# Kernel optimization log

Hardware: AMD Instinct MI355X
Metric: run time of the kernel (lower is better)

Reference implementation:

```python
import jax, jax.numpy as jnp
from jax import lax
import numpy as np

B, H, W = 1, 128, 256
C = 32           # feature_channels
D = 32           # max_disp
HID = 64         # hidden_channels in message passing
ITERS = 5


def conv2d(x, w, b):
    # x: [N, Cin, H, W], w: [Cout, Cin, kh, kw], SAME padding, stride 1
    y = lax.conv_general_dilated(x, w, (1, 1), [(1, 1), (1, 1)],
                                 dimension_numbers=('NCHW', 'OIHW', 'NCHW'))
    return y + b[None, :, None, None]


def setup_inputs() -> dict:
    key = jax.random.key(0)
    ks = jax.random.split(key, 12)
    def p(k, shape, s=0.05):
        return jax.random.normal(k, shape, jnp.float32) * s
    return {
        'left_img':  jax.random.normal(ks[0], (B, 3, H, W), jnp.float32),
        'right_img': jax.random.normal(ks[1], (B, 3, H, W), jnp.float32),
        # feature extractor (3 -> C -> C)
        'fe_w1': p(ks[2], (C, 3, 3, 3)),  'fe_b1': jnp.zeros((C,), jnp.float32),
        'fe_w2': p(ks[3], (C, C, 3, 3)),  'fe_b2': jnp.zeros((C,), jnp.float32),
        # cost volume 1x1 conv over concat(left, shifted_right): 2C -> 1
        'cv_w': p(ks[4], (2 * C,)),       'cv_b': jnp.zeros((), jnp.float32),
        # message passing: concat(feature, belief)=C+1 -> HID -> 1
        'mp_w1': p(ks[5], (HID, C + 1, 3, 3)), 'mp_b1': jnp.zeros((HID,), jnp.float32),
        'mp_w2': p(ks[6], (1, HID, 3, 3)),     'mp_b2': jnp.zeros((1,), jnp.float32),
        # refinement: concat(left_img, disparity)=4 -> 32 -> 32 -> 1 residual
        'rf_w1': p(ks[7], (32, 4, 3, 3)),  'rf_b1': jnp.zeros((32,), jnp.float32),
        'rf_w2': p(ks[8], (32, 32, 3, 3)), 'rf_b2': jnp.zeros((32,), jnp.float32),
        'rf_w3': p(ks[9], (1, 32, 3, 3)),  'rf_b3': jnp.zeros((1,), jnp.float32),
    }


def _forward(left_img, right_img, fe_w1, fe_b1, fe_w2, fe_b2, cv_w, cv_b,
             mp_w1, mp_b1, mp_w2, mp_b2, rf_w1, rf_b1, rf_w2, rf_b2, rf_w3, rf_b3):
    def feat(img):
        h = jax.nn.relu(conv2d(img, fe_w1, fe_b1))
        return jax.nn.relu(conv2d(h, fe_w2, fe_b2))

    lf = feat(left_img)    # [B, C, H, W]
    rf = feat(right_img)   # [B, C, H, W]

    # Cost volume: shift right features by each disparity, 1x1 conv on concat.
    rf_sh = jnp.stack([jnp.pad(rf, ((0, 0), (0, 0), (0, 0), (d, 0)))[..., :W]
                       for d in range(D)])                     # [D, B, C, H, W]
    pair = jnp.concatenate([jnp.broadcast_to(lf[None], rf_sh.shape), rf_sh], axis=2)  # [D,B,2C,H,W]
    cost = jnp.einsum('dbchw,c->dbhw', pair, cv_w) + cv_b      # [D, B, H, W]
    data = cost[:, :, None]                                     # [D, B, 1, H, W]

    # Iterative BP message passing, vectorized across all disparity planes.
    def mp(data_term):  # data_term: [B, 1, H, W]
        def step(belief, _):
            x = jnp.concatenate([lf, belief], axis=1)           # [B, C+1, H, W]
            hdn = jax.nn.relu(conv2d(x, mp_w1, mp_b1))          # [B, HID, H, W]
            msg = conv2d(hdn, mp_w2, mp_b2)                     # [B, 1, H, W]
            return data_term + msg, None
        belief, _ = lax.scan(step, data_term, None, length=ITERS)
        return belief

    beliefs = jax.vmap(mp)(data)                                # [D, B, 1, H, W]
    refined = jnp.transpose(beliefs, (1, 2, 0, 3, 4))           # [B, 1, D, H, W]

    prob = jax.nn.softmax(-refined, axis=2)                     # [B, 1, D, H, W]
    idx = jnp.arange(D, dtype=prob.dtype)
    disparity = jnp.einsum('bodhw,d->bohw', prob, idx)          # [B, 1, H, W]

    # Refinement network (residual).
    x = jnp.concatenate([left_img, disparity], axis=1)          # [B, 4, H, W]
    r = jax.nn.relu(conv2d(x, rf_w1, rf_b1))
    r = jax.nn.relu(conv2d(r, rf_w2, rf_b2))
    res = conv2d(r, rf_w3, rf_b3)
    return disparity + res                                      # [B, 1, H, W]


def reference(left_img, right_img, fe_w1, fe_b1, fe_w2, fe_b2, cv_w, cv_b,
              mp_w1, mp_b1, mp_w2, mp_b2, rf_w1, rf_b1, rf_w2, rf_b2, rf_w3, rf_b3):
    return _forward(left_img, right_img, fe_w1, fe_b1, fe_w2, fe_b2, cv_w, cv_b,
                    mp_w1, mp_b1, mp_w2, mp_b2, rf_w1, rf_b1, rf_w2, rf_b2, rf_w3, rf_b3)
```

## Files before the change

kernel.cpp:

```cpp
#include <hip/hip_runtime.h>
#include <hip/hip_bf16.h>

#define H 128
#define W 256
#define HW (H*W)
#define NC 32
#define ND 32
#define NHID 64

__global__ __launch_bounds__(256) void conv3x3(
        const float* __restrict__ in0, const float* __restrict__ in1,
        float* __restrict__ out0, float* __restrict__ out1,
        const float* __restrict__ w, const float* __restrict__ b,
        int CIN, int COUT, int wstride, int dorelu,
        const float* __restrict__ addin) {
    __shared__ float wS[2304];
    __shared__ float tile[2][4][10][35];
    const int tid = threadIdx.x;
    const int zg = (COUT + 7) >> 3;
    const int img = blockIdx.z / zg;
    const int cog = blockIdx.z % zg;
    const float* in = img ? in1 : in0;
    float* out = img ? out1 : out0;
    const int cobase = cog * 8;
    int nco = COUT - cobase; if (nco > 8) nco = 8;
    const int gx0 = blockIdx.x * 32, gy0 = blockIdx.y * 8;
    const int tx = tid & 31, ty = tid >> 5;

    const int wcnt = nco * CIN * 9;
    for (int i = tid; i < wcnt; i += 256) {
        int co = i / (CIN * 9), rem = i % (CIN * 9);
        wS[i] = w[(size_t)(cobase + co) * wstride + rem];
    }

    const int nst = (CIN + 3) >> 2;
    {
        int nch = CIN < 4 ? CIN : 4;
        for (int i = tid; i < nch * 340; i += 256) {
            int ch = i / 340, rem = i % 340;
            int r = rem / 34, cc = rem % 34;
            int gy = gy0 + r - 1, gx = gx0 + cc - 1;
            tile[0][ch][r][cc] = (gy >= 0 && gy < H && gx >= 0 && gx < W)
                                 ? in[(size_t)ch * HW + gy * W + gx] : 0.f;
        }
    }
    __syncthreads();

    float acc[8];
#pragma unroll
    for (int i = 0; i < 8; i++) acc[i] = 0.f;

    for (int s = 0; s < nst; s++) {
        const int c0 = s * 4;
        int nch = CIN - c0; if (nch > 4) nch = 4;
        if (s + 1 < nst) {
            const int c1 = c0 + 4;
            int nch2 = CIN - c1; if (nch2 > 4) nch2 = 4;
            const int nb = (s + 1) & 1;
            for (int i = tid; i < nch2 * 340; i += 256) {
                int ch = i / 340, rem = i % 340;
                int r = rem / 34, cc = rem % 34;
                int gy = gy0 + r - 1, gx = gx0 + cc - 1;
                tile[nb][ch][r][cc] = (gy >= 0 && gy < H && gx >= 0 && gx < W)
                                      ? in[(size_t)(c1 + ch) * HW + gy * W + gx] : 0.f;
            }
        }
        const int cb = s & 1;
        for (int ch = 0; ch < nch; ch++) {
            float v[9];
#pragma unroll
            for (int ky = 0; ky < 3; ky++)
#pragma unroll
                for (int kx = 0; kx < 3; kx++)
                    v[ky * 3 + kx] = tile[cb][ch][ty + ky][tx + kx];
            const int wb = (c0 + ch) * 9;
#pragma unroll
            for (int co = 0; co < 8; co++) {
                if (co < nco) {
                    const float* wp = &wS[co * CIN * 9 + wb];
#pragma unroll
                    for (int k = 0; k < 9; k++) acc[co] += wp[k] * v[k];
                }
            }
        }
        __syncthreads();
    }

    const int gy = gy0 + ty, gx = gx0 + tx;
    const float ad = addin ? addin[gy * W + gx] : 0.f;
#pragma unroll
    for (int co = 0; co < 8; co++) {
        if (co < nco) {
            float r = acc[co] + b[cobase + co];
            if (dorelu) r = fmaxf(r, 0.f);
            r += ad;
            out[(size_t)(cobase + co) * HW + gy * W + gx] = r;
        }
    }
}

__global__ void chan_dot(const float* __restrict__ lf, const float* __restrict__ rf,
                         const float* __restrict__ cvw,
                         float* __restrict__ lsum, float* __restrict__ rsum) {
    int p = blockIdx.x * 256 + threadIdx.x;
    if (p >= HW) return;
    float ls = 0.f, rs = 0.f;
    for (int c = 0; c < NC; c++) {
        ls += lf[c * HW + p] * cvw[c];
        rs += rf[c * HW + p] * cvw[NC + c];
    }
    lsum[p] = ls;
    rsum[p] = rs;
}

__global__ void cost_expand(const float* __restrict__ lsum, const float* __restrict__ rsum,
                            const float* __restrict__ cvb,
                            float* __restrict__ cost, float* __restrict__ bel) {
    int idx = blockIdx.x * 256 + threadIdx.x;
    if (idx >= ND * HW) return;
    int d = idx / HW, p = idx % HW;
    int col = p & (W - 1);
    float c = lsum[p] + cvb[0];
    if (col >= d) c += rsum[p - d];
    cost[idx] = c;
    bel[idx] = c;
}

__global__ void a_transpose(const float* __restrict__ A, float* __restrict__ At) {
    __shared__ float t[64][65];
    int p0 = blockIdx.x * 64;
    int tx = threadIdx.x & 63;
    int ty = threadIdx.x >> 6;
#pragma unroll
    for (int r = 0; r < 16; r++) {
        int hid = ty * 16 + r;
        t[tx][hid] = A[(size_t)hid * HW + p0 + tx];
    }
    __syncthreads();
#pragma unroll
    for (int r = 0; r < 16; r++) {
        int p = ty * 16 + r;
        At[(size_t)(p0 + p) * 64 + tx] = t[p][tx];
    }
}

#define LOADROW(YC, AR)                                                        \
  {                                                                            \
    if ((YC) >= 0 && (YC) < H) {                                               \
      AR[0] = bp[e0off];                                                       \
      _Pragma("unroll") for (int j = 1; j < 17; j++) AR[j] = bp[(j - 8) * 64]; \
      AR[17] = bp[e17off];                                                     \
    }                                                                          \
    bp += W * 64;                                                              \
  }

#define COMPUTE(U, AR, HARR)                                                   \
  {                                                                            \
    const int yc_ = y0 + (U);                                                  \
    if (yc_ < 0 || yc_ >= H) {                                                 \
      _Pragma("unroll") for (int j = 0; j < 18; j++) HARR[j] = 0.f;            \
    } else {                                                                   \
      float bw_[3][3];                                                         \
      _Pragma("unroll") for (int r = 0; r < 3; r++) {                          \
        bw_[r][0] = belW[(U) + 1 + r][0];                                      \
        bw_[r][1] = belW[(U) + 1 + r][1];                                      \
      }                                                                        \
      _Pragma("unroll") for (int j = 0; j < 18; j++) {                         \
        float acc_ = AR[j];                                                    \
        _Pragma("unroll") for (int r = 0; r < 3; r++)                          \
          bw_[r][(j + 2) % 3] = belW[(U) + 1 + r][j + 2];                      \
        _Pragma("unroll") for (int r = 0; r < 3; r++)                          \
          _Pragma("unroll") for (int c = 0; c < 3; c++)                        \
            acc_ += w1[r * 3 + c] * bw_[r][(j + c) % 3];                       \
        HARR[j] = fmaxf(acc_, 0.f);                                            \
      }                                                                        \
      if (x0 == 0) HARR[0] = 0.f;                                              \
      if (x0 == W - 16) HARR[17] = 0.f;                                        \
    }                                                                          \
  }

#define EMIT3(T, HH2, HH1, HH0)                                                \
  {                                                                            \
    _Pragma("unroll") for (int jo = 0; jo < 16; jo++) {                        \
      float pp = w2[0] * HH2[jo] + w2[1] * HH2[jo + 1] + w2[2] * HH2[jo + 2]   \
               + w2[3] * HH1[jo] + w2[4] * HH1[jo + 1] + w2[5] * HH1[jo + 2]   \
               + w2[6] * HH0[jo] + w2[7] * HH0[jo + 1] + w2[8] * HH0[jo + 2];  \
      partW[jo][lane] = pp;                                                    \
    }                                                                          \
    asm volatile("s_waitcnt lgkmcnt(0)" ::: "memory");                         \
    {                                                                          \
      const float4* pr = (const float4*)&partW[pq][qq * 16];                   \
      float4 v0 = pr[0], v1 = pr[1], v2 = pr[2], v3 = pr[3];                   \
      float s_ = (((v0.x + v0.y) + (v0.z + v0.w)) +                            \
                  ((v1.x + v1.y) + (v1.z + v1.w))) +                           \
                 (((v2.x + v2.y) + (v2.z + v2.w)) +                            \
                  ((v3.x + v3.y) + (v3.z + v3.w)));                            \
      s_ += __shfl_xor(s_, 16);                                                \
      s_ += __shfl_xor(s_, 32);                                                \
      if (qq == 0)                                                             \
        bout[obase + (size_t)(T) * W] = costW[(T)][pq] + s_ + b2;              \
      asm volatile("s_waitcnt lgkmcnt(0)" ::: "memory");                       \
    }                                                                          \
  }

#define STEP(T, AIN, AOUT, HX2, HX1, HX0, DOLOAD)                              \
  {                                                                            \
    if (DOLOAD) { LOADROW(y0 + (T) + 2, AOUT); }                               \
    COMPUTE((T) + 1, AIN, HX0);                                                \
    EMIT3(T, HX2, HX1, HX0);                                                   \
  }

__global__ __launch_bounds__(256, 1) void mp_iter_fast(
    const float* __restrict__ At,
    const float* __restrict__ cost,
    const float* __restrict__ bin,
    float* __restrict__ bout,
    const float* __restrict__ mp_w1,
    const float* __restrict__ mp_w2,
    const float* __restrict__ mp_b2) {
    __shared__ float belS[4][20][20];
    __shared__ float costS[4][16][16];
    __shared__ float partS[4][16][68];

    const int tid = threadIdx.x;
    const int lane = tid & 63;
    const int lw = tid >> 6;
    float (*belW)[20]  = belS[lw];
    float (*costW)[16] = costS[lw];
    float (*partW)[68] = partS[lw];

    const int i = blockIdx.x;
    const int xcd = i & 7;
    const int jj = i >> 3;
    const int sl = jj & 15;
    const int d4 = jj >> 4;
    const int strip = xcd * 16 + sl;
    const int d = d4 * 4 + lw;
    const int x0 = (strip & 15) * 16;
    const int y0 = (strip >> 4) * 16;

    float w1[9], w2[9];
#pragma unroll
    for (int k = 0; k < 9; k++) {
        w1[k] = mp_w1[lane * 297 + 288 + k];
        w2[k] = mp_w2[lane * 9 + k];
    }
    const float b2 = mp_b2[0];

    const float* bp = At + (size_t)(y0 - 1) * (W * 64) + (x0 + 7) * 64 + lane;
    const int e0off  = (x0 == 0)      ? -448 : -512;
    const int e17off = (x0 == W - 16) ?  512 :  576;

    const float* beld = bin + (size_t)d * HW;
#pragma unroll
    for (int it = 0; it < 7; it++) {
        int idx = it * 64 + lane;
        if (idx < 400) {
            int r = idx / 20, c = idx % 20;
            int gy = y0 - 2 + r, gx = x0 - 2 + c;
            belW[r][c] = (gy >= 0 && gy < H && gx >= 0 && gx < W) ? beld[gy * W + gx] : 0.f;
        }
    }
#pragma unroll
    for (int it = 0; it < 4; it++) {
        int idx = it * 64 + lane;
        int r = idx >> 4, c = idx & 15;
        costW[r][c] = cost[(size_t)d * HW + (size_t)(y0 + r) * W + x0 + c];
    }
    asm volatile("s_waitcnt lgkmcnt(0)" ::: "memory");

    const int pq = lane & 15, qq = lane >> 4;
    const size_t obase = (size_t)d * HW + (size_t)y0 * W + x0 + pq;

    float aA[18], aB[18];
    float hA[18], hB[18], hC[18];

    LOADROW(y0 - 1, aA);
    LOADROW(y0, aB);
    COMPUTE(-1, aA, hA);
    LOADROW(y0 + 1, aA);
    COMPUTE(0, aB, hB);

    STEP(0,  aA, aB, hA, hB, hC, 1)
    STEP(1,  aB, aA, hB, hC, hA, 1)
    STEP(2,  aA, aB, hC, hA, hB, 1)
    STEP(3,  aB, aA, hA, hB, hC, 1)
    STEP(4,  aA, aB, hB, hC, hA, 1)
    STEP(5,  aB, aA, hC, hA, hB, 1)
    STEP(6,  aA, aB, hA, hB, hC, 1)
    STEP(7,  aB, aA, hB, hC, hA, 1)
    STEP(8,  aA, aB, hC, hA, hB, 1)
    STEP(9,  aB, aA, hA, hB, hC, 1)
    STEP(10, aA, aB, hB, hC, hA, 1)
    STEP(11, aB, aA, hC, hA, hB, 1)
    STEP(12, aA, aB, hA, hB, hC, 1)
    STEP(13, aB, aA, hB, hC, hA, 1)
    STEP(14, aA, aB, hC, hA, hB, 1)
    STEP(15, aB, aA, hA, hB, hC, 0)
}

__global__ void softmax_disp(const float* __restrict__ bel, const float* __restrict__ left,
                             float* __restrict__ disp, float* __restrict__ x4) {
    int p = blockIdx.x * 256 + threadIdx.x;
    if (p >= HW) return;
    float v[ND];
    float m = -1e30f;
#pragma unroll
    for (int d = 0; d < ND; d++) {
        v[d] = -bel[d * HW + p];
        m = fmaxf(m, v[d]);
    }
    float s = 0.f, ws = 0.f;
#pragma unroll
    for (int d = 0; d < ND; d++) {
        float e = __expf(v[d] - m);
        s += e;
        ws += e * (float)d;
    }
    float dv = ws / s;
    disp[p] = dv;
    x4[3 * HW + p] = dv;
    x4[p] = left[p];
    x4[HW + p] = left[HW + p];
    x4[2 * HW + p] = left[2 * HW + p];
}

extern "C" void kernel_launch(void* const* d_in, const int* in_sizes, int n_in,
                              void* d_out, int out_size, void* d_ws, size_t ws_size,
                              hipStream_t stream) {
    const float* left   = (const float*)d_in[0];
    const float* right  = (const float*)d_in[1];
    const float* fe_w1  = (const float*)d_in[2];
    const float* fe_b1  = (const float*)d_in[3];
    const float* fe_w2  = (const float*)d_in[4];
    const float* fe_b2  = (const float*)d_in[5];
    const float* cv_w   = (const float*)d_in[6];
    const float* cv_b   = (const float*)d_in[7];
    const float* mp_w1  = (const float*)d_in[8];
    const float* mp_b1  = (const float*)d_in[9];
    const float* mp_w2  = (const float*)d_in[10];
    const float* mp_b2  = (const float*)d_in[11];
    const float* rf_w1  = (const float*)d_in[12];
    const float* rf_b1  = (const float*)d_in[13];
    const float* rf_w2  = (const float*)d_in[14];
    const float* rf_b2  = (const float*)d_in[15];
    const float* rf_w3  = (const float*)d_in[16];
    const float* rf_b3  = (const float*)d_in[17];
    float* out = (float*)d_out;

    float* ws = (float*)d_ws;
    float* At    = ws;
    float* tmp0  = ws;
    float* tmp1  = ws + 1048576;
    float* lf    = ws + 2097152;
    float* rfeat = ws + 3145728;
    float* cost  = ws + 4194304;
    float* Araw  = ws + 4194304;
    float* bel   = ws + 5242880;
    float* bel2  = ws + 6291456;
    float* lsum  = ws + 7340032;
    float* rsum  = ws + 7372800;
    float* disp  = ws + 7405568;
    float* x4    = ws + 7438336;

    dim3 blk(256);

    conv3x3<<<dim3(8, 16, 8), blk, 0, stream>>>(left, right, tmp0, tmp1, fe_w1, fe_b1, 3, 32, 27, 1, nullptr);
    conv3x3<<<dim3(8, 16, 8), blk, 0, stream>>>(tmp0, tmp1, lf, rfeat, fe_w2, fe_b2, 32, 32, 288, 1, nullptr);

    chan_dot<<<dim3(HW / 256), blk, 0, stream>>>(lf, rfeat, cv_w, lsum, rsum);

    conv3x3<<<dim3(8, 16, 8), blk, 0, stream>>>(lf, lf, Araw, Araw, mp_w1, mp_b1, 32, 64, 297, 0, nullptr);
    a_transpose<<<dim3(HW / 64), blk, 0, stream>>>(Araw, At);

    cost_expand<<<dim3(ND * HW / 256), blk, 0, stream>>>(lsum, rsum, cv_b, cost, bel);

    dim3 gmp(1024);
    mp_iter_fast<<<gmp, blk, 0, stream>>>(At, cost, bel,  bel2, mp_w1, mp_w2, mp_b2);
    mp_iter_fast<<<gmp, blk, 0, stream>>>(At, cost, bel2, bel,  mp_w1, mp_w2, mp_b2);
    mp_iter_fast<<<gmp, blk, 0, stream>>>(At, cost, bel,  bel2, mp_w1, mp_w2, mp_b2);
    mp_iter_fast<<<gmp, blk, 0, stream>>>(At, cost, bel2, bel,  mp_w1, mp_w2, mp_b2);
    mp_iter_fast<<<gmp, blk, 0, stream>>>(At, cost, bel,  bel2, mp_w1, mp_w2, mp_b2);

    softmax_disp<<<dim3(HW / 256), blk, 0, stream>>>(bel2, left, disp, x4);

    conv3x3<<<dim3(8, 16, 4), blk, 0, stream>>>(x4, x4, At, At, rf_w1, rf_b1, 4, 32, 36, 1, nullptr);
    conv3x3<<<dim3(8, 16, 4), blk, 0, stream>>>(At, At, rfeat, rfeat, rf_w2, rf_b2, 32, 32, 288, 1, nullptr);
    conv3x3<<<dim3(8, 16, 1), blk, 0, stream>>>(rfeat, rfeat, out, out, rf_w3, rf_b3, 32, 1, 288, 0, disp);
}
```

Before: 553.5 us.

## Software-pipeline message-passing row reduction with double-buffered LDS partials

Restructures the per-row loop of the message-passing kernel so the LDS partial sums for row T-1 are read and reduced while row T+2's hidden activations are computed and the next A row is loaded. Partial buffers are double-buffered by row parity, and the explicit lgkmcnt waits are removed. The goal is to hide LDS and reduction latency behind ALU work. It also vectorises the cost tile load, shifts the A row base pointer by one column with adjusted offsets, and raises launch bounds to request two blocks per CU. The risks are more register pressure and relying on the compiler to order LDS accesses correctly without the explicit waits.

```diff
diff --git a/kernel.cpp b/kernel.cpp
--- a/kernel.cpp
+++ b/kernel.cpp
@@ -148,7 +148,7 @@
   {                                                                            \
     if ((YC) >= 0 && (YC) < H) {                                               \
       AR[0] = bp[e0off];                                                       \
-      _Pragma("unroll") for (int j = 1; j < 17; j++) AR[j] = bp[(j - 8) * 64]; \
+      _Pragma("unroll") for (int j = 1; j < 17; j++) AR[j] = bp[(j - 9) * 64]; \
       AR[17] = bp[e17off];                                                     \
     }                                                                          \
     bp += W * 64;                                                              \
@@ -179,38 +179,43 @@
     }                                                                          \
   }
 
-#define EMIT3(T, HH2, HH1, HH0)                                                \
+#define WRITES(T, HM, H0, HP)                                                  \
   {                                                                            \
     _Pragma("unroll") for (int jo = 0; jo < 16; jo++) {                        \
-      float pp = w2[0] * HH2[jo] + w2[1] * HH2[jo + 1] + w2[2] * HH2[jo + 2]   \
-               + w2[3] * HH1[jo] + w2[4] * HH1[jo + 1] + w2[5] * HH1[jo + 2]   \
-               + w2[6] * HH0[jo] + w2[7] * HH0[jo + 1] + w2[8] * HH0[jo + 2];  \
-      partW[jo][lane] = pp;                                                    \
+      float pp = w2[0] * HM[jo] + w2[1] * HM[jo + 1] + w2[2] * HM[jo + 2]      \
+               + w2[3] * H0[jo] + w2[4] * H0[jo + 1] + w2[5] * H0[jo + 2]      \
+               + w2[6] * HP[jo] + w2[7] * HP[jo + 1] + w2[8] * HP[jo + 2];     \
+      partW[(T) & 1][jo][lane] = pp;                                           \
     }                                                                          \
-    asm volatile("s_waitcnt lgkmcnt(0)" ::: "memory");                         \
-    {                                                                          \
-      const float4* pr = (const float4*)&partW[pq][qq * 16];                   \
-      float4 v0 = pr[0], v1 = pr[1], v2 = pr[2], v3 = pr[3];                   \
-      float s_ = (((v0.x + v0.y) + (v0.z + v0.w)) +                            \
-                  ((v1.x + v1.y) + (v1.z + v1.w))) +                           \
-                 (((v2.x + v2.y) + (v2.z + v2.w)) +                            \
-                  ((v3.x + v3.y) + (v3.z + v3.w)));                            \
-      s_ += __shfl_xor(s_, 16);                                                \
-      s_ += __shfl_xor(s_, 32);                                                \
-      if (qq == 0)                                                             \
-        bout[obase + (size_t)(T) * W] = costW[(T)][pq] + s_ + b2;              \
-      asm volatile("s_waitcnt lgkmcnt(0)" ::: "memory");                       \
-    }                                                                          \
-  }
-
-#define STEP(T, AIN, AOUT, HX2, HX1, HX0, DOLOAD)                              \
-  {                                                                            \
-    if (DOLOAD) { LOADROW(y0 + (T) + 2, AOUT); }                               \
-    COMPUTE((T) + 1, AIN, HX0);                                                \
-    EMIT3(T, HX2, HX1, HX0);                                                   \
-  }
-
-__global__ __launch_bounds__(256, 1) void mp_iter_fast(
+  }
+
+#define RISSUE(T)                                                              \
+  {                                                                            \
+    const float4* pr_ = (const float4*)&partW[(T) & 1][pq][qq * 16];           \
+    rv0 = pr_[0]; rv1 = pr_[1]; rv2 = pr_[2]; rv3 = pr_[3];                    \
+  }
+
+#define RFINISH(T)                                                             \
+  {                                                                            \
+    float s_ = (((rv0.x + rv0.y) + (rv0.z + rv0.w)) +                          \
+                ((rv1.x + rv1.y) + (rv1.z + rv1.w))) +                         \
+               (((rv2.x + rv2.y) + (rv2.z + rv2.w)) +                          \
+                ((rv3.x + rv3.y) + (rv3.z + rv3.w)));                          \
+    s_ += __shfl_xor(s_, 16);                                                  \
+    s_ += __shfl_xor(s_, 32);                                                  \
+    if (qq == 0) bout[obase + (size_t)(T) * W] = costW[(T)][pq] + s_ + b2;     \
+  }
+
+#define STEPG(T, HM, H0, HP, AIN, AOUT, DOLOAD)                                \
+  {                                                                            \
+    WRITES(T, HM, H0, HP);                                                     \
+    RISSUE((T) - 1);                                                           \
+    if (DOLOAD) { LOADROW(y0 + (T) + 3, AOUT); }                               \
+    COMPUTE((T) + 2, AIN, HM);                                                 \
+    RFINISH((T) - 1);                                                          \
+  }
+
+__global__ __launch_bounds__(256, 2) void mp_iter_fast(
     const float* __restrict__ At,
     const float* __restrict__ cost,
     const float* __restrict__ bin,
@@ -220,14 +225,14 @@
     const float* __restrict__ mp_b2) {
     __shared__ float belS[4][20][20];
     __shared__ float costS[4][16][16];
-    __shared__ float partS[4][16][68];
+    __shared__ float partS[4][2][16][68];
 
     const int tid = threadIdx.x;
     const int lane = tid & 63;
     const int lw = tid >> 6;
     float (*belW)[20]  = belS[lw];
     float (*costW)[16] = costS[lw];
-    float (*partW)[68] = partS[lw];
+    float (*partW)[16][68] = partS[lw];
 
     const int i = blockIdx.x;
     const int xcd = i & 7;
@@ -247,9 +252,9 @@
     }
     const float b2 = mp_b2[0];
 
-    const float* bp = At + (size_t)(y0 - 1) * (W * 64) + (x0 + 7) * 64 + lane;
-    const int e0off  = (x0 == 0)      ? -448 : -512;
-    const int e17off = (x0 == W - 16) ?  512 :  576;
+    const float* bp = At + (size_t)(y0 - 1) * (W * 64) + (x0 + 8) * 64 + lane;
+    const int e0off  = (x0 == 0)      ? -512 : -576;
+    const int e17off = (x0 == W - 16) ?  448 :  512;
 
     const float* beld = bin + (size_t)d * HW;
 #pragma unroll
@@ -261,42 +266,48 @@
             belW[r][c] = (gy >= 0 && gy < H && gx >= 0 && gx < W) ? beld[gy * W + gx] : 0.f;
         }
     }
-#pragma unroll
-    for (int it = 0; it < 4; it++) {
-        int idx = it * 64 + lane;
-        int r = idx >> 4, c = idx & 15;
-        costW[r][c] = cost[(size_t)d * HW + (size_t)(y0 + r) * W + x0 + c];
-    }
-    asm volatile("s_waitcnt lgkmcnt(0)" ::: "memory");
+    {
+        int r = lane >> 2, cg = lane & 3;
+        float4 cv = *(const float4*)&cost[(size_t)d * HW + (size_t)(y0 + r) * W + x0 + cg * 4];
+        *(float4*)&costW[r][cg * 4] = cv;
+    }
 
     const int pq = lane & 15, qq = lane >> 4;
     const size_t obase = (size_t)d * HW + (size_t)y0 * W + x0 + pq;
 
     float aA[18], aB[18];
     float hA[18], hB[18], hC[18];
+    float4 rv0, rv1, rv2, rv3;
 
     LOADROW(y0 - 1, aA);
-    LOADROW(y0, aB);
+    LOADROW(y0,     aB);
     COMPUTE(-1, aA, hA);
     LOADROW(y0 + 1, aA);
     COMPUTE(0, aB, hB);
-
-    STEP(0,  aA, aB, hA, hB, hC, 1)
-    STEP(1,  aB, aA, hB, hC, hA, 1)
-    STEP(2,  aA, aB, hC, hA, hB, 1)
-    STEP(3,  aB, aA, hA, hB, hC, 1)
-    STEP(4,  aA, aB, hB, hC, hA, 1)
-    STEP(5,  aB, aA, hC, hA, hB, 1)
-    STEP(6,  aA, aB, hA, hB, hC, 1)
-    STEP(7,  aB, aA, hB, hC, hA, 1)
-    STEP(8,  aA, aB, hC, hA, hB, 1)
-    STEP(9,  aB, aA, hA, hB, hC, 1)
-    STEP(10, aA, aB, hB, hC, hA, 1)
-    STEP(11, aB, aA, hC, hA, hB, 1)
-    STEP(12, aA, aB, hA, hB, hC, 1)
-    STEP(13, aB, aA, hB, hC, hA, 1)
-    STEP(14, aA, aB, hC, hA, hB, 1)
-    STEP(15, aB, aA, hA, hB, hC, 0)
+    LOADROW(y0 + 2, aB);
+    COMPUTE(1, aA, hC);
+    WRITES(0, hA, hB, hC);
+    LOADROW(y0 + 3, aA);
+    COMPUTE(2, aB, hA);
+    STEPG(1,  hB, hC, hA, aA, aB, 1)
+    STEPG(2,  hC, hA, hB, aB, aA, 1)
+    STEPG(3,  hA, hB, hC, aA, aB, 1)
+    STEPG(4,  hB, hC, hA, aB, aA, 1)
+    STEPG(5,  hC, hA, hB, aA, aB, 1)
+    STEPG(6,  hA, hB, hC, aB, aA, 1)
+    STEPG(7,  hB, hC, hA, aA, aB, 1)
+    STEPG(8,  hC, hA, hB, aB, aA, 1)
+    STEPG(9,  hA, hB, hC, aA, aB, 1)
+    STEPG(10, hB, hC, hA, aB, aA, 1)
+    STEPG(11, hC, hA, hB, aA, aB, 1)
+    STEPG(12, hA, hB, hC, aB, aA, 1)
+    STEPG(13, hB, hC, hA, aA, aB, 1)
+    STEPG(14, hC, hA, hB, aB, aA, 0)
+    WRITES(15, hA, hB, hC);
+    RISSUE(14);
+    RFINISH(14);
+    RISSUE(15);
+    RFINISH(15);
 }
 
 __global__ void softmax_disp(const float* __restrict__ bel, const float* __restrict__ left,
```

Result: slower. 584.5 us (+5.6%).
